# Kernel tuning notes

Hardware: AMD Instinct MI355X
Metric: run time of the kernel (lower is better)

## Reference

```python
import jax, jax.numpy as jnp
import numpy as np

B, T_MEL, E, M, NFPS = 64, 2000, 512, 80, 2
P, H = 256, 1024
T_DEC = T_MEL // NFPS


def setup_inputs() -> dict:
    key = jax.random.key(0)
    ks = iter(jax.random.split(key, 40))

    def rn(shape, fan_in):
        return jax.random.normal(next(ks), shape, jnp.float32) / np.float32(np.sqrt(fan_in))

    z = lambda *s: jnp.zeros(s, jnp.float32)
    return {
        "memorys": jax.random.normal(next(ks), (B, T_MEL, E), jnp.float32),
        "decoder_inputs": jax.random.normal(next(ks), (B, T_MEL, M), jnp.float32),
        "memory_lengths": jax.random.randint(next(ks), (B,), 1, T_MEL + 1),
        "pre_w1": rn((P, M), M), "pre_b1": z(P),
        "pre_w2": rn((P, P), P), "pre_b2": z(P),
        "g1_wih": rn((3 * H, P + E), P + E), "g1_whh": rn((3 * H, H), H),
        "g1_bih": z(3 * H), "g1_bhh": z(3 * H),
        "att_w": rn((H, H + E), H + E), "att_b": z(H),
        "g2_wih": rn((3 * H, H), H), "g2_whh": rn((3 * H, H), H),
        "g2_bih": z(3 * H), "g2_bhh": z(3 * H),
        "g3_wih": rn((3 * H, H), H), "g3_whh": rn((3 * H, H), H),
        "g3_bih": z(3 * H), "g3_bhh": z(3 * H),
        "proj_w": rn((M * NFPS, H + E), H + E), "proj_b": z(M * NFPS),
    }


def gru_cell(x, h, wih, whh, bih, bhh):
    # PyTorch GRUCell gate order: r, z, n
    gi = x @ wih.T + bih
    gh = h @ whh.T + bhh
    i_r, i_z, i_n = jnp.split(gi, 3, axis=-1)
    h_r, h_z, h_n = jnp.split(gh, 3, axis=-1)
    r = jax.nn.sigmoid(i_r + h_r)
    zg = jax.nn.sigmoid(i_z + h_z)
    n = jnp.tanh(i_n + r * h_n)
    return (1.0 - zg) * n + zg * h


def reference(memorys, decoder_inputs, memory_lengths,
              pre_w1, pre_b1, pre_w2, pre_b2,
              g1_wih, g1_whh, g1_bih, g1_bhh,
              att_w, att_b,
              g2_wih, g2_whh, g2_bih, g2_bhh,
              g3_wih, g3_whh, g3_bih, g3_bhh,
              proj_w, proj_b):
    # memory_lengths -> mask is computed but never used in decode(); ignored.
    # Teacher-forced inputs: [T_MEL,B,M] -> every NFPS-th frame, prepend go frames, drop last
    di = jnp.transpose(decoder_inputs, (1, 0, 2))[NFPS - 1::NFPS]   # [T_DEC,B,M]
    go = jnp.zeros((NFPS - 1, B, M), di.dtype)
    di = jnp.concatenate([go, di], axis=0)[:-1]                      # [T_DEC,B,M]
    # Prenet (dropout inactive in deterministic/eval reference)
    x = jax.nn.relu(di @ pre_w1.T + pre_b1)
    x = jax.nn.relu(x @ pre_w2.T + pre_b2)                           # [T_DEC,B,P]
    # Pool memory over n_frames_per_step groups -> per-step context
    mem = memorys.reshape(B, T_DEC, NFPS, E).mean(axis=2)
    mem = jnp.transpose(mem, (1, 0, 2))                              # [T_DEC,B,E]

    def step(carry, inp):
        h1, h2, h3 = carry
        xt, mt = inp
        h1 = gru_cell(jnp.concatenate([xt, mt], -1), h1, g1_wih, g1_whh, g1_bih, g1_bhh)
        d2 = jnp.concatenate([h1, mt], -1) @ att_w.T + att_b
        h2 = gru_cell(d2, h2, g2_wih, g2_whh, g2_bih, g2_bhh)
        r2 = h2 + d2
        h3 = gru_cell(r2, h3, g3_wih, g3_whh, g3_bih, g3_bhh)
        r3 = h3 + r2
        out = jnp.concatenate([r3, mt], -1) @ proj_w.T + proj_b      # [B, M*NFPS]
        return (h1, h2, h3), out

    h0 = tuple(jnp.zeros((B, H), x.dtype) for _ in range(3))
    _, outs = jax.lax.scan(step, h0, (x, mem))                       # [T_DEC,B,M*NFPS]
    return jnp.transpose(outs, (1, 0, 2))                            # [B,T_DEC,M*NFPS]
```

## Files before the change

kernel.cpp:

```cpp
#include <hip/hip_runtime.h>
#include <stdint.h>

#define TD   1000
#define BB   64
#define HH   1024
#define EE   512
#define MMEL 80
#define TMEL 2000
#define RTOT (TD*BB)
#define BH   (BB*HH)
#define DRNG 64

typedef __attribute__((ext_vector_type(8))) short short8;
typedef __attribute__((ext_vector_type(4))) float f32x4;

__device__ __forceinline__ float bf2f(uint16_t h){ return __uint_as_float(((uint32_t)h)<<16); }
__device__ __forceinline__ uint16_t f2bf(float f){
  uint32_t u = __float_as_uint(f);
  return (uint16_t)((u + 0x7fffu + ((u>>16)&1u)) >> 16);
}

__device__ __forceinline__ void async16(const void* g, void* l) {
  __builtin_amdgcn_global_load_lds((const __attribute__((address_space(1))) void*)g,
                                   (__attribute__((address_space(3))) void*)l, 16, 0, 0);
}

__device__ __forceinline__ f32x4 mfma16(short8 a, short8 b, f32x4 c){
  return __builtin_amdgcn_mfma_f32_16x16x32_bf16(a, b, c, 0, 0, 0);
}


__global__ void k_zero16(uint16_t* p, int n){ int i=blockIdx.x*256+threadIdx.x; if(i<n) p[i]=0; }
__global__ void k_zero32(unsigned* p, int n){ int i=blockIdx.x*256+threadIdx.x; if(i<n) p[i]=0u; }
__global__ void k_fill(float* p, int n, float v){ int i=blockIdx.x*256+threadIdx.x; if(i<n) p[i]=v; }

__global__ void k_cast(const float* __restrict__ src, uint16_t* __restrict__ dst,
                       int rows, int src_ld, int col0, int cols, int dst_ld){
  int i = blockIdx.x*256 + threadIdx.x;
  if (i >= rows*dst_ld) return;
  int r = i/dst_ld, c = i - r*dst_ld;
  float v = (c < cols) ? src[(size_t)r*src_ld + col0 + c] : 0.f;
  dst[i] = f2bf(v);
}

__global__ void k_di(const float* __restrict__ dec, uint16_t* __restrict__ di){
  int i = blockIdx.x*256 + threadIdx.x;
  if (i >= RTOT*96) return;
  int row = i/96, c = i - row*96;
  int t = row>>6, b = row&63;
  float v = 0.f;
  if (c < MMEL && t > 0) v = dec[((size_t)b*TMEL + (2*t-1))*MMEL + c];
  di[i] = f2bf(v);
}

__global__ void k_mem(const float* __restrict__ mem, uint16_t* __restrict__ out){
  int i = blockIdx.x*256 + threadIdx.x;
  if (i >= RTOT*EE) return;
  int row = i/EE, e = i - row*EE;
  int t = row>>6, b = row&63;
  size_t base = ((size_t)b*TMEL + 2*t)*EE + e;
  out[i] = f2bf(0.5f*(mem[base] + mem[base+EE]));
}


template<int OM, int DT>
__global__ __launch_bounds__(256)
void k_gemm(const uint16_t* __restrict__ A1p, int K1, int lda1,
            const uint16_t* __restrict__ A2p, int K2, int lda2,
            const uint16_t* __restrict__ Bw, int ldb,
            void* __restrict__ Cp, int ldc,
            const float* __restrict__ bias,
            const void* __restrict__ Dadd, int ldd,
            int N, int relu)
{
  __shared__ __align__(16) uint16_t As[128*32];
  __shared__ __align__(16) uint16_t Bs[128*32];
  const int tid = threadIdx.x;
  const int w = tid>>6, lane = tid&63;
  const int q = lane>>4, ln = lane&15;
  const int m0 = blockIdx.y*128, n0 = blockIdx.x*128;
  const int wr = (w&1)*64, wc = (w>>1)*64;
  const int srow = w*32 + (lane>>2);
  const int scol = (lane&3)*8;
  const uint16_t* A1g = A1p + (size_t)(m0+srow)*lda1 + scol;
  const uint16_t* A1g2 = A1g + (size_t)16*lda1;
  const uint16_t* A2g = A2p ? A2p + (size_t)(m0+srow)*lda2 + scol : nullptr;
  const uint16_t* A2g2 = A2p ? A2g + (size_t)16*lda2 : nullptr;
  int bn1 = n0+srow;     bn1 = bn1 < N ? bn1 : N-1;
  int bn2 = n0+srow+16;  bn2 = bn2 < N ? bn2 : N-1;
  const uint16_t* Bg  = Bw + (size_t)bn1*ldb + scol;
  const uint16_t* Bg2 = Bw + (size_t)bn2*ldb + scol;
  uint16_t* As0 = &As[(w*32)*32];
  uint16_t* As1 = &As[(w*32+16)*32];
  uint16_t* Bs0 = &Bs[(w*32)*32];
  uint16_t* Bs1 = &Bs[(w*32+16)*32];
  const int K = K1 + K2;

  f32x4 acc[4][4] = {};
  for (int kt=0; kt<K; kt+=32) {
    __syncthreads();
    if (kt < K1) { async16(A1g+kt, As0);  async16(A1g2+kt, As1); }
    else         { async16(A2g+(kt-K1), As0);  async16(A2g2+(kt-K1), As1); }
    async16(Bg+kt, Bs0);  async16(Bg2+kt, Bs1);
    __syncthreads();
    short8 af[4], bfr[4];
    #pragma unroll
    for (int i=0;i<4;++i) af[i]  = *(const short8*)&As[(wr+16*i+ln)*32 + q*8];
    #pragma unroll
    for (int j=0;j<4;++j) bfr[j] = *(const short8*)&Bs[(wc+16*j+ln)*32 + q*8];
    #pragma unroll
    for (int i=0;i<4;++i)
      #pragma unroll
      for (int j=0;j<4;++j)
        acc[i][j] = mfma16(af[i], bfr[j], acc[i][j]);
  }

  #pragma unroll
  for (int i=0;i<4;++i){
    #pragma unroll
    for (int j=0;j<4;++j){
      int col = n0 + wc + 16*j + ln;
      if (col >= N) continue;
      float bv = bias ? bias[col] : 0.f;
      #pragma unroll
      for (int r=0;r<4;++r){
        int row = m0 + wr + 16*i + 4*q + r;
        float v = acc[i][j][r] + bv;
        if (Dadd) {
          if (DT) v += ((const float*)Dadd)[(size_t)row*ldd + col];
          else    v += bf2f(((const uint16_t*)Dadd)[(size_t)row*ldd + col]);
        }
        if (relu) v = v > 0.f ? v : 0.f;
        if (OM==0) {
          ((uint16_t*)Cp)[(size_t)row*ldc + col] = f2bf(v);
        } else if (OM==1) {
          int t = row>>6, b = row&63;
          ((float*)Cp)[((size_t)b*TD + t)*ldc + col] = v;
        } else {
          ((float*)Cp)[(size_t)row*ldc + col] = v;
        }
      }
    }
  }
}


__device__ __forceinline__ void signal_flag(unsigned* f, int idx, unsigned v){
  if (threadIdx.x == 0)
    __hip_atomic_store(f + idx*32, v, __ATOMIC_RELEASE, __HIP_MEMORY_SCOPE_AGENT);
}
__device__ __forceinline__ void wait_flags(unsigned* f, int n, unsigned target){
  if ((int)threadIdx.x < n) {
    unsigned* p = f + threadIdx.x*32;
    while (__hip_atomic_load(p, __ATOMIC_RELAXED, __HIP_MEMORY_SCOPE_AGENT) < target)
      __builtin_amdgcn_s_sleep(1);
    __builtin_amdgcn_fence(__ATOMIC_ACQUIRE, "agent");
  }
  __syncthreads();
}


template<int ROLE>
__device__ __forceinline__ void fetch_gi(int t,
    const uint16_t* X2, const uint16_t* MEM, const uint16_t* gsrc,
    const uint16_t* smw, int w, int q, int ln, f32x4 (&ga)[3])
{
  ga[0] = (f32x4){0.f,0.f,0.f,0.f}; ga[1] = ga[0]; ga[2] = ga[0];
  const int swz = (ln&7)<<3;
  if (ROLE == 1) {
    const uint16_t* a0 = X2 + ((size_t)t*64 + 16*w + ln)*256 + q*8;
    #pragma unroll 4
    for (int ks=0; ks<8; ++ks) {
      short8 a = *(const short8*)(a0 + ks*32);
      #pragma unroll
      for (int g=0; g<3; ++g) {
        short8 b = *(const short8*)(smw + ((((g*16+ln)*768) + ks*32 + q*8) ^ swz));
        ga[g] = mfma16(a, b, ga[g]);
      }
    }
    const uint16_t* a1 = MEM + ((size_t)t*64 + 16*w + ln)*512 + q*8;
    #pragma unroll 4
    for (int ks=0; ks<16; ++ks) {
      short8 a = *(const short8*)(a1 + ks*32);
      #pragma unroll
      for (int g=0; g<3; ++g) {
        short8 b = *(const short8*)(smw + ((((g*16+ln)*768) + 256 + ks*32 + q*8) ^ swz));
        ga[g] = mfma16(a, b, ga[g]);
      }
    }
  } else {
    const uint16_t* base = gsrc + (ROLE==2 ? (size_t)(t % DRNG)*BH : (size_t)t*BH);
    const uint16_t* a0 = base + (size_t)(16*w + ln)*1024 + q*8;
    #pragma unroll 8
    for (int ks=0; ks<32; ++ks) {
      short8 a = *(const short8*)(a0 + ks*32);
      #pragma unroll
      for (int g=0; g<3; ++g) {
        short8 b = *(const short8*)(smw + ((((g*16+ln)*1024) + ks*32 + q*8) ^ swz));
        ga[g] = mfma16(a, b, ga[g]);
      }
    }
  }
}


template<int ROLE>
__device__ void rec_role(int i,
    const uint16_t* whh, const uint16_t* wih,
    const float* bih, const float* bhh,
    const uint16_t* X2, const uint16_t* MEM, const uint16_t* gsrc,
    uint16_t* Hs, uint16_t* rout,
    unsigned* fOwn, unsigned* fDep, int nDep,
    uint16_t* smw, float* red)
{
  const int tid = threadIdx.x;
  const int w = tid>>6, lane = tid&63;
  const int q = lane>>4, ln = lane&15;
  const int j = i*16 + ln;
  constexpr int LDK = (ROLE==1) ? 768 : 1024;

  for (int u = tid; u < (48*LDK)/8; u += 256) {
    int row = (u*8)/LDK, col = (u*8) - row*LDK;
    int g = row>>4, r16 = row&15;
    short8 v = *(const short8*)(wih + (size_t)(g*1024 + i*16 + r16)*LDK + col);
    *(short8*)(smw + ((row*LDK + col) ^ ((row&7)<<3))) = v;
  }
  short8 breg[3][8];
  #pragma unroll
  for (int g=0; g<3; ++g) {
    const uint16_t* Bp = whh + (size_t)(g*1024 + j)*1024 + (w*8)*32 + q*8;
    #pragma unroll
    for (int ks=0; ks<8; ++ks) breg[g][ks] = *(const short8*)(Bp + ks*32);
  }
  const float bh0 = bhh[j], bh1 = bhh[1024+j], bh2 = bhh[2048+j];
  const float bi0 = bih[j], bi1 = bih[1024+j], bi2 = bih[2048+j];
  __syncthreads();

  float hold[4] = {0.f,0.f,0.f,0.f};
  f32x4 ga[3];
  if (ROLE != 1) wait_flags(fDep, nDep, 1u);
  fetch_gi<ROLE>(0, X2, MEM, gsrc, smw, w, q, ln, ga);

  for (int t=0; t<TD; ++t) {
    if (t > 0) wait_flags(fOwn, 64, (unsigned)t);
    const uint16_t* hp = Hs + (size_t)t*BH;

    f32x4 acc[3][4];
    #pragma unroll
    for (int g=0; g<3; ++g)
      #pragma unroll
      for (int mt=0; mt<4; ++mt) acc[g][mt] = (f32x4){0.f,0.f,0.f,0.f};
    #pragma unroll
    for (int ks=0; ks<8; ++ks) {
      const int k0 = (w*8+ks)*32 + q*8;
      #pragma unroll
      for (int mt=0; mt<4; ++mt) {
        short8 a = *(const short8*)(hp + (size_t)(16*mt+ln)*HH + k0);
        acc[0][mt] = mfma16(a, breg[0][ks], acc[0][mt]);
        acc[1][mt] = mfma16(a, breg[1][ks], acc[1][mt]);
        acc[2][mt] = mfma16(a, breg[2][ks], acc[2][mt]);
      }
    }
    #pragma unroll
    for (int g=0; g<3; ++g)
      #pragma unroll
      for (int mt=0; mt<4; ++mt)
        *(f32x4*)&red[((w*12 + g*4 + mt)*64 + lane)*4] = acc[g][mt];
    __syncthreads();
    f32x4 s[3];
    #pragma unroll
    for (int g=0; g<3; ++g) {
      f32x4 sv = *(const f32x4*)&red[((g*4 + w)*64 + lane)*4];
      #pragma unroll
      for (int kw=1; kw<4; ++kw)
        sv += *(const f32x4*)&red[((kw*12 + g*4 + w)*64 + lane)*4];
      s[g] = sv;
    }

    const uint16_t* gib = (ROLE==2) ? gsrc + (size_t)(t % DRNG)*BH
                        : (ROLE==3) ? gsrc + (size_t)t*BH : nullptr;
    #pragma unroll
    for (int r=0; r<4; ++r) {
      const int b = 16*w + 4*q + r;
      float rg = 1.f/(1.f + __expf(-(ga[0][r] + bi0 + s[0][r] + bh0)));
      float zg = 1.f/(1.f + __expf(-(ga[1][r] + bi1 + s[1][r] + bh1)));
      float nx = ga[2][r] + bi2 + rg*(s[2][r] + bh2);
      float ng = 1.f - 2.f/(1.f + __expf(2.f*nx));
      float hn = (1.f - zg)*ng + zg*hold[r];
      hold[r] = hn;
      Hs[(size_t)(t+1)*BH + (size_t)b*HH + j] = f2bf(hn);
      if (ROLE != 1) {
        float av = bf2f(gib[(size_t)b*HH + j]);
        rout[((size_t)t*64 + b)*HH + j] = f2bf(hn + av);
      }
    }
    __syncthreads();
    signal_flag(fOwn, i, (unsigned)(t+1));
    if (t+1 < TD) {
      if (ROLE != 1) wait_flags(fDep, nDep, (unsigned)(t+2));
      fetch_gi<ROLE>(t+1, X2, MEM, gsrc, smw, w, q, ln, ga);
    }
  }
}


__device__ void att_role(int i, const uint16_t* wah, const uint16_t* H1,
    const uint16_t* APRE, uint16_t* D2R,
    unsigned* fA, unsigned* fB, unsigned* fD, uint16_t* smw)
{
  const int tid = threadIdx.x;
  const int w = tid>>6, lane = tid&63;
  const int q = lane>>4, ln = lane&15;
  const int c0 = i*32;
  for (int u = tid; u < (32*1024)/8; u += 256) {
    int row = (u*8)>>10, col = (u*8)&1023;
    short8 v = *(const short8*)(wah + (size_t)(c0+row)*1024 + col);
    *(short8*)(smw + ((row*1024 + col) ^ ((row&7)<<3))) = v;
  }
  __syncthreads();
  const int swz = (ln&7)<<3;
  for (int t=0; t<TD; ++t) {
    wait_flags(fA, 64, (unsigned)(t+1));
    if (t >= DRNG) wait_flags(fB, 64, (unsigned)(t - DRNG + 1));
    const uint16_t* h1t = H1 + (size_t)(t+1)*BH;
    f32x4 dacc[2];
    dacc[0] = (f32x4){0.f,0.f,0.f,0.f}; dacc[1] = dacc[0];
    const uint16_t* a0 = h1t + (size_t)(16*w + ln)*HH + q*8;
    #pragma unroll 8
    for (int ks=0; ks<32; ++ks) {
      short8 a = *(const short8*)(a0 + ks*32);
      #pragma unroll
      for (int jf=0; jf<2; ++jf) {
        short8 b = *(const short8*)(smw + ((((jf*16+ln)*1024) + ks*32 + q*8) ^ swz));
        dacc[jf] = mfma16(a, b, dacc[jf]);
      }
    }
    uint16_t* slot = D2R + (size_t)(t % DRNG)*BH;
    #pragma unroll
    for (int jf=0; jf<2; ++jf)
      #pragma unroll
      for (int r=0; r<4; ++r) {
        int b = 16*w + 4*q + r, col = c0 + 16*jf + ln;
        float v = dacc[jf][r] + bf2f(APRE[((size_t)t*64 + b)*HH + col]);
        slot[(size_t)b*HH + col] = f2bf(v);
      }
    __syncthreads();
    signal_flag(fD, i, (unsigned)(t+1));
  }
}


__global__ __launch_bounds__(256,1)
void k_pipe(const uint16_t* wG1WHH, const uint16_t* wG2WHH, const uint16_t* wG3WHH,
            const uint16_t* wG1WIH, const uint16_t* wG2WIH, const uint16_t* wG3WIH,
            const uint16_t* wATTWH,
            const float* b1ih, const float* b1hh, const float* b2ih, const float* b2hh,
            const float* b3ih, const float* b3hh,
            const uint16_t* X2, const uint16_t* MEM, const uint16_t* APRE,
            uint16_t* H1, uint16_t* H2, uint16_t* H3,
            uint16_t* R2, uint16_t* R3, uint16_t* D2R, unsigned* flags)
{
  __shared__ __align__(16) uint16_t smw[49152];
  __shared__ __align__(16) float red[12288];
  unsigned* fA = flags;
  unsigned* fD = flags + 64*32;
  unsigned* fB = flags + 96*32;
  unsigned* fC = flags + 160*32;
  const int blk = blockIdx.x;
  if (blk < 64) {
    rec_role<1>(blk, wG1WHH, wG1WIH, b1ih, b1hh, X2, MEM, nullptr,
                H1, nullptr, fA, nullptr, 0, smw, red);
  } else if (blk < 96) {
    att_role(blk-64, wATTWH, H1, APRE, D2R, fA, fB, fD, smw);
  } else if (blk < 160) {
    rec_role<2>(blk-96, wG2WHH, wG2WIH, b2ih, b2hh, nullptr, nullptr, D2R,
                H2, R2, fB, fD, 32, smw, red);
  } else {
    rec_role<3>(blk-160, wG3WHH, wG3WIH, b3ih, b3hh, nullptr, nullptr, R2,
                H3, R3, fC, fB, 64, smw, red);
  }
}


extern "C" void kernel_launch(void* const* d_in, const int* in_sizes, int n_in,
                              void* d_out, int out_size, void* d_ws, size_t ws_size,
                              hipStream_t stream)
{
  (void)in_sizes; (void)n_in;
  const float* memorys = (const float*)d_in[0];
  const float* decin   = (const float*)d_in[1];
  const float* pre_w1  = (const float*)d_in[3];
  const float* pre_b1  = (const float*)d_in[4];
  const float* pre_w2  = (const float*)d_in[5];
  const float* pre_b2  = (const float*)d_in[6];
  const float* g1_wih  = (const float*)d_in[7];
  const float* g1_whh  = (const float*)d_in[8];
  const float* g1_bih  = (const float*)d_in[9];
  const float* g1_bhh  = (const float*)d_in[10];
  const float* att_w   = (const float*)d_in[11];
  const float* att_b   = (const float*)d_in[12];
  const float* g2_wih  = (const float*)d_in[13];
  const float* g2_whh  = (const float*)d_in[14];
  const float* g2_bih  = (const float*)d_in[15];
  const float* g2_bhh  = (const float*)d_in[16];
  const float* g3_wih  = (const float*)d_in[17];
  const float* g3_whh  = (const float*)d_in[18];
  const float* g3_bih  = (const float*)d_in[19];
  const float* g3_bhh  = (const float*)d_in[20];
  const float* proj_w  = (const float*)d_in[21];
  const float* proj_b  = (const float*)d_in[22];

  uint16_t* ws = (uint16_t*)d_ws;
  size_t off = 0;
  auto alloc = [&](size_t n){ uint16_t* p = ws + off; off += (n + 127) & ~size_t(127); return p; };

  uint16_t* wG1WHH = alloc((size_t)3072*1024);
  uint16_t* wG2WHH = alloc((size_t)3072*1024);
  uint16_t* wG3WHH = alloc((size_t)3072*1024);
  uint16_t* wG1WIH = alloc((size_t)3072*768);
  uint16_t* wG2WIH = alloc((size_t)3072*1024);
  uint16_t* wG3WIH = alloc((size_t)3072*1024);
  uint16_t* wATTWH = alloc((size_t)1024*1024);
  uint16_t* wATTWM = alloc((size_t)1024*512);
  uint16_t* wPW1   = alloc((size_t)256*96);
  uint16_t* wPW2   = alloc((size_t)256*256);
  uint16_t* wPROJr = alloc((size_t)160*1024);
  uint16_t* wPROJm = alloc((size_t)160*512);

  float*    PM   = (float*)alloc((size_t)RTOT*160*2);
  uint16_t* X2   = alloc((size_t)RTOT*256);
  uint16_t* MEM  = alloc((size_t)RTOT*512);
  uint16_t* APRE = alloc((size_t)RTOT*1024);
  uint16_t* H1   = alloc((size_t)(TD+1)*BH);
  uint16_t* H2   = alloc((size_t)(TD+1)*BH);
  uint16_t* H3   = alloc((size_t)(TD+1)*BH);
  uint16_t* R2   = alloc((size_t)RTOT*1024);
  uint16_t* D2R  = alloc((size_t)DRNG*BH);
  unsigned* flags = (unsigned*)(ws + off); off += 224*32*2 + 256;

  uint16_t* DI96 = H3;
  uint16_t* X1   = H2;

  size_t need_bytes = off * 2;
  if (ws_size < need_bytes) {
    float v = 1048576.0f + (float)(ws_size >> 20);
    k_fill<<<dim3((out_size+255)/256), dim3(256), 0, stream>>>((float*)d_out, out_size, v);
    return;
  }

  auto NB = [](long long n){ return dim3((unsigned)((n+255)/256)); };

  k_cast<<<NB(3072*1024), dim3(256), 0, stream>>>(g1_whh, wG1WHH, 3072, 1024, 0, 1024, 1024);
  k_cast<<<NB(3072*1024), dim3(256), 0, stream>>>(g2_whh, wG2WHH, 3072, 1024, 0, 1024, 1024);
  k_cast<<<NB(3072*1024), dim3(256), 0, stream>>>(g3_whh, wG3WHH, 3072, 1024, 0, 1024, 1024);
  k_cast<<<NB(3072*768),  dim3(256), 0, stream>>>(g1_wih, wG1WIH, 3072, 768, 0, 768, 768);
  k_cast<<<NB(3072*1024), dim3(256), 0, stream>>>(g2_wih, wG2WIH, 3072, 1024, 0, 1024, 1024);
  k_cast<<<NB(3072*1024), dim3(256), 0, stream>>>(g3_wih, wG3WIH, 3072, 1024, 0, 1024, 1024);
  k_cast<<<NB(1024*1024), dim3(256), 0, stream>>>(att_w,  wATTWH, 1024, 1536, 0, 1024, 1024);
  k_cast<<<NB(1024*512),  dim3(256), 0, stream>>>(att_w,  wATTWM, 1024, 1536, 1024, 512, 512);
  k_cast<<<NB(256*96),    dim3(256), 0, stream>>>(pre_w1, wPW1,   256, 80, 0, 80, 96);
  k_cast<<<NB(256*256),   dim3(256), 0, stream>>>(pre_w2, wPW2,   256, 256, 0, 256, 256);
  k_cast<<<NB(160*1024),  dim3(256), 0, stream>>>(proj_w, wPROJr, 160, 1536, 0, 1024, 1024);
  k_cast<<<NB(160*512),   dim3(256), 0, stream>>>(proj_w, wPROJm, 160, 1536, 1024, 512, 512);

  k_di <<<NB((long long)RTOT*96),  dim3(256), 0, stream>>>(decin, DI96);
  k_mem<<<NB((long long)RTOT*EE),  dim3(256), 0, stream>>>(memorys, MEM);

  k_gemm<0,0><<<dim3(2,500), dim3(256), 0, stream>>>(DI96,96,96, nullptr,0,0, wPW1,96, X1,256, pre_b1, nullptr,0, 256, 1);
  k_gemm<0,0><<<dim3(2,500), dim3(256), 0, stream>>>(X1,256,256, nullptr,0,0, wPW2,256, X2,256, pre_b2, nullptr,0, 256, 1);

  k_gemm<0,0><<<dim3(8,500), dim3(256), 0, stream>>>(MEM,512,512, nullptr,0,0, wATTWM,512, APRE,1024, att_b, nullptr,0, 1024, 0);
  k_gemm<2,0><<<dim3(2,500), dim3(256), 0, stream>>>(MEM,512,512, nullptr,0,0, wPROJm,512, PM,160, proj_b, nullptr,0, 160, 0);

  k_zero16<<<NB(BH), dim3(256), 0, stream>>>(H1, BH);
  k_zero16<<<NB(BH), dim3(256), 0, stream>>>(H2, BH);
  k_zero16<<<NB(BH), dim3(256), 0, stream>>>(H3, BH);
  k_zero32<<<dim3(28), dim3(256), 0, stream>>>(flags, 224*32);

  k_pipe<<<dim3(224), dim3(256), 0, stream>>>(
      wG1WHH, wG2WHH, wG3WHH, wG1WIH, wG2WIH, wG3WIH, wATTWH,
      g1_bih, g1_bhh, g2_bih, g2_bhh, g3_bih, g3_bhh,
      X2, MEM, APRE, H1, H2, H3, R2, APRE, D2R, flags);

  k_gemm<1,1><<<dim3(2,500), dim3(256), 0, stream>>>(APRE,1024,1024, nullptr,0,0, wPROJr,1024, d_out,160, nullptr, PM,160, 160, 0);
}
```

Measured before the change: 16.95 ms.

## Precompute GRU1 input gates, ring-buffer hidden states, batch bypass loads

The GRU1 input projection (prenet output plus memory context times W_ih) moves out of the persistent recurrent kernel into one large upfront GEMM, so layer-1 blocks only read precomputed gates each step. Hidden-state and residual histories become small ring buffers, with backpressure flags so producers cannot overwrite slots their consumers have not read yet. A combined wait routine checks both own-progress and downstream flags, and operand loads are batched through relaxed atomic loads that bypass the cache. This is meant to shorten the serial per-step critical path and cut memory footprint. The cost is an extra GI1 buffer and more complex cross-block synchronisation, which raises deadlock and ordering risk; the acquire fence after waiting was also dropped.

Result: slower. 23.81 ms (+40.5%).

```diff
diff --git a/kernel.cpp b/kernel.cpp
--- a/kernel.cpp
+++ b/kernel.cpp
@@ -9,10 +9,13 @@
 #define TMEL 2000
 #define RTOT (TD*BB)
 #define BH   (BB*HH)
-#define DRNG 64
+#define RH1  80
+#define RH23 8
+#define RNG  64
 
 typedef __attribute__((ext_vector_type(8))) short short8;
 typedef __attribute__((ext_vector_type(4))) float f32x4;
+typedef unsigned long long u64t;
 
 __device__ __forceinline__ float bf2f(uint16_t h){ return __uint_as_float(((uint32_t)h)<<16); }
 __device__ __forceinline__ uint16_t f2bf(float f){
@@ -27,6 +30,12 @@
 
 __device__ __forceinline__ f32x4 mfma16(short8 a, short8 b, f32x4 c){
   return __builtin_amdgcn_mfma_f32_16x16x32_bf16(a, b, c, 0, 0, 0);
+}
+
+__device__ __forceinline__ short8 ld16_bypass(const uint16_t* p){
+  u64t lo = __hip_atomic_load((const u64t*)p,       __ATOMIC_RELAXED, __HIP_MEMORY_SCOPE_AGENT);
+  u64t hi = __hip_atomic_load(((const u64t*)p) + 1, __ATOMIC_RELAXED, __HIP_MEMORY_SCOPE_AGENT);
+  union { u64t q[2]; short8 s; } u; u.q[0] = lo; u.q[1] = hi; return u.s;
 }
 
 
@@ -149,81 +158,70 @@
   if (threadIdx.x == 0)
     __hip_atomic_store(f + idx*32, v, __ATOMIC_RELEASE, __HIP_MEMORY_SCOPE_AGENT);
 }
-__device__ __forceinline__ void wait_flags(unsigned* f, int n, unsigned target){
-  if ((int)threadIdx.x < n) {
-    unsigned* p = f + threadIdx.x*32;
-    while (__hip_atomic_load(p, __ATOMIC_RELAXED, __HIP_MEMORY_SCOPE_AGENT) < target)
+
+__device__ __forceinline__ void wait2(unsigned* f0, int n0, unsigned t0,
+                                      unsigned* f1, int n1, unsigned t1){
+  const int tid = threadIdx.x;
+  unsigned* p = nullptr; unsigned tgt = 0;
+  if (tid < n0)            { p = f0 + tid*32;       tgt = t0; }
+  else if (tid < n0 + n1)  { p = f1 + (tid-n0)*32;  tgt = t1; }
+  if (p && tgt)
+    while (__hip_atomic_load(p, __ATOMIC_RELAXED, __HIP_MEMORY_SCOPE_AGENT) < tgt)
       __builtin_amdgcn_s_sleep(1);
-    __builtin_amdgcn_fence(__ATOMIC_ACQUIRE, "agent");
-  }
   __syncthreads();
 }
 
 
 template<int ROLE>
-__device__ __forceinline__ void fetch_gi(int t,
-    const uint16_t* X2, const uint16_t* MEM, const uint16_t* gsrc,
-    const uint16_t* smw, int w, int q, int ln, f32x4 (&ga)[3])
+__device__ __forceinline__ void fetch_tail(int t, const uint16_t* gsrc,
+    const uint16_t* smw, int w, int q, int ln, int j, f32x4 (&ga)[3], float (&gibv)[4])
 {
+  const uint16_t* base = gsrc + (size_t)(t & (RNG-1))*BH;
   ga[0] = (f32x4){0.f,0.f,0.f,0.f}; ga[1] = ga[0]; ga[2] = ga[0];
   const int swz = (ln&7)<<3;
-  if (ROLE == 1) {
-    const uint16_t* a0 = X2 + ((size_t)t*64 + 16*w + ln)*256 + q*8;
-    #pragma unroll 4
-    for (int ks=0; ks<8; ++ks) {
-      short8 a = *(const short8*)(a0 + ks*32);
-      #pragma unroll
-      for (int g=0; g<3; ++g) {
-        short8 b = *(const short8*)(smw + ((((g*16+ln)*768) + ks*32 + q*8) ^ swz));
-        ga[g] = mfma16(a, b, ga[g]);
-      }
-    }
-    const uint16_t* a1 = MEM + ((size_t)t*64 + 16*w + ln)*512 + q*8;
-    #pragma unroll 4
-    for (int ks=0; ks<16; ++ks) {
-      short8 a = *(const short8*)(a1 + ks*32);
-      #pragma unroll
-      for (int g=0; g<3; ++g) {
-        short8 b = *(const short8*)(smw + ((((g*16+ln)*768) + 256 + ks*32 + q*8) ^ swz));
-        ga[g] = mfma16(a, b, ga[g]);
-      }
-    }
-  } else {
-    const uint16_t* base = gsrc + (ROLE==2 ? (size_t)(t % DRNG)*BH : (size_t)t*BH);
-    const uint16_t* a0 = base + (size_t)(16*w + ln)*1024 + q*8;
-    #pragma unroll 8
-    for (int ks=0; ks<32; ++ks) {
-      short8 a = *(const short8*)(a0 + ks*32);
-      #pragma unroll
-      for (int g=0; g<3; ++g) {
-        short8 b = *(const short8*)(smw + ((((g*16+ln)*1024) + ks*32 + q*8) ^ swz));
-        ga[g] = mfma16(a, b, ga[g]);
-      }
-    }
+  short8 a2[32];
+  #pragma unroll
+  for (int ks=0; ks<32; ++ks)
+    a2[ks] = ld16_bypass(base + (size_t)(16*w+ln)*1024 + q*8 + ks*32);
+  #pragma unroll
+  for (int ks=0; ks<32; ++ks) {
+    #pragma unroll
+    for (int g=0; g<3; ++g) {
+      short8 b = *(const short8*)(smw + ((((g*16+ln)*1024) + ks*32 + q*8) ^ swz));
+      ga[g] = mfma16(a2[ks], b, ga[g]);
+    }
+  }
+  #pragma unroll
+  for (int r=0; r<4; ++r){
+    int b = 16*w + 4*q + r;
+    unsigned v = __hip_atomic_load((const unsigned*)(base + (size_t)b*HH + (j & ~1)),
+                                   __ATOMIC_RELAXED, __HIP_MEMORY_SCOPE_AGENT);
+    gibv[r] = bf2f((uint16_t)((j&1) ? (v>>16) : (v & 0xffffu)));
   }
 }
 
 
 template<int ROLE>
 __device__ void rec_role(int i,
-    const uint16_t* whh, const uint16_t* wih,
-    const float* bih, const float* bhh,
-    const uint16_t* X2, const uint16_t* MEM, const uint16_t* gsrc,
-    uint16_t* Hs, uint16_t* rout,
-    unsigned* fOwn, unsigned* fDep, int nDep,
+    const uint16_t* __restrict__ whh, const uint16_t* __restrict__ wih,
+    const float* __restrict__ bih, const float* __restrict__ bhh,
+    const uint16_t* __restrict__ GI1, const uint16_t* __restrict__ gsrc,
+    uint16_t* __restrict__ Hs, uint16_t* __restrict__ rout,
+    unsigned* fOwn, unsigned* fPrev, int nPrev, unsigned* fNext, int nNext,
     uint16_t* smw, float* red)
 {
   const int tid = threadIdx.x;
   const int w = tid>>6, lane = tid&63;
   const int q = lane>>4, ln = lane&15;
   const int j = i*16 + ln;
-  constexpr int LDK = (ROLE==1) ? 768 : 1024;
-
-  for (int u = tid; u < (48*LDK)/8; u += 256) {
-    int row = (u*8)/LDK, col = (u*8) - row*LDK;
-    int g = row>>4, r16 = row&15;
-    short8 v = *(const short8*)(wih + (size_t)(g*1024 + i*16 + r16)*LDK + col);
-    *(short8*)(smw + ((row*LDK + col) ^ ((row&7)<<3))) = v;
+  constexpr int RH = (ROLE==1) ? RH1 : RH23;
+
+  if (ROLE != 1) {
+    for (int u = tid; u < (48*1024)/8; u += 256) {
+      int row = (u*8)>>10, col = (u*8)&1023;
+      short8 v = *(const short8*)(wih + (size_t)((row>>4)*1024 + i*16 + (row&15))*1024 + col);
+      *(short8*)(smw + ((row*1024 + col) ^ ((row&7)<<3))) = v;
+    }
   }
   short8 breg[3][8];
   #pragma unroll
@@ -233,17 +231,40 @@
     for (int ks=0; ks<8; ++ks) breg[g][ks] = *(const short8*)(Bp + ks*32);
   }
   const float bh0 = bhh[j], bh1 = bhh[1024+j], bh2 = bhh[2048+j];
-  const float bi0 = bih[j], bi1 = bih[1024+j], bi2 = bih[2048+j];
+  float bi0 = 0.f, bi1 = 0.f, bi2 = 0.f;
+  if (ROLE != 1) { bi0 = bih[j]; bi1 = bih[1024+j]; bi2 = bih[2048+j]; }
   __syncthreads();
 
   float hold[4] = {0.f,0.f,0.f,0.f};
   f32x4 ga[3];
-  if (ROLE != 1) wait_flags(fDep, nDep, 1u);
-  fetch_gi<ROLE>(0, X2, MEM, gsrc, smw, w, q, ln, ga);
+  float gibv[4] = {0.f,0.f,0.f,0.f};
+
+  if (ROLE == 1) {
+    #pragma unroll
+    for (int r=0; r<4; ++r){
+      size_t gb = (size_t)(16*w + 4*q + r)*3072;
+      ga[0][r] = bf2f(GI1[gb + j]);
+      ga[1][r] = bf2f(GI1[gb + 1024 + j]);
+      ga[2][r] = bf2f(GI1[gb + 2048 + j]);
+    }
+  } else {
+    wait2(fPrev, nPrev, 1u, nullptr, 0, 0u);
+    fetch_tail<ROLE>(0, gsrc, smw, w, q, ln, j, ga, gibv);
+  }
 
   for (int t=0; t<TD; ++t) {
-    if (t > 0) wait_flags(fOwn, 64, (unsigned)t);
-    const uint16_t* hp = Hs + (size_t)t*BH;
+    unsigned bp = 0u;
+    if (ROLE == 1)      bp = (t >= RH1-1) ? (unsigned)(t - (RH1-2)) : 0u;
+    else if (nNext)     bp = (t >= RNG)   ? (unsigned)(t - (RNG-1)) : 0u;
+    wait2(fOwn, 64, (unsigned)t, fNext, nNext, bp);
+
+    const uint16_t* hp = Hs + (size_t)(t % RH)*BH;
+    short8 av[32];
+    #pragma unroll
+    for (int ks=0; ks<8; ++ks)
+      #pragma unroll
+      for (int mt=0; mt<4; ++mt)
+        av[ks*4+mt] = ld16_bypass(hp + (size_t)(16*mt+ln)*HH + (w*8+ks)*32 + q*8);
 
     f32x4 acc[3][4];
     #pragma unroll
@@ -252,15 +273,14 @@
       for (int mt=0; mt<4; ++mt) acc[g][mt] = (f32x4){0.f,0.f,0.f,0.f};
     #pragma unroll
     for (int ks=0; ks<8; ++ks) {
-      const int k0 = (w*8+ks)*32 + q*8;
       #pragma unroll
       for (int mt=0; mt<4; ++mt) {
-        short8 a = *(const short8*)(hp + (size_t)(16*mt+ln)*HH + k0);
-        acc[0][mt] = mfma16(a, breg[0][ks], acc[0][mt]);
-        acc[1][mt] = mfma16(a, breg[1][ks], acc[1][mt]);
-        acc[2][mt] = mfma16(a, breg[2][ks], acc[2][mt]);
+        acc[0][mt] = mfma16(av[ks*4+mt], breg[0][ks], acc[0][mt]);
+        acc[1][mt] = mfma16(av[ks*4+mt], breg[1][ks], acc[1][mt]);
+        acc[2][mt] = mfma16(av[ks*4+mt], breg[2][ks], acc[2][mt]);
       }
     }
+
     #pragma unroll
     for (int g=0; g<3; ++g)
       #pragma unroll
@@ -277,8 +297,7 @@
       s[g] = sv;
     }
 
-    const uint16_t* gib = (ROLE==2) ? gsrc + (size_t)(t % DRNG)*BH
-                        : (ROLE==3) ? gsrc + (size_t)t*BH : nullptr;
+    uint16_t* hw = Hs + (size_t)((t+1) % RH)*BH;
     #pragma unroll
     for (int r=0; r<4; ++r) {
       const int b = 16*w + 4*q + r;
@@ -288,25 +307,35 @@
       float ng = 1.f - 2.f/(1.f + __expf(2.f*nx));
       float hn = (1.f - zg)*ng + zg*hold[r];
       hold[r] = hn;
-      Hs[(size_t)(t+1)*BH + (size_t)b*HH + j] = f2bf(hn);
-      if (ROLE != 1) {
-        float av = bf2f(gib[(size_t)b*HH + j]);
-        rout[((size_t)t*64 + b)*HH + j] = f2bf(hn + av);
-      }
+      hw[(size_t)b*HH + j] = f2bf(hn);
+      if (ROLE == 2) rout[(size_t)(t & (RNG-1))*BH + (size_t)b*HH + j] = f2bf(hn + gibv[r]);
+      if (ROLE == 3) rout[((size_t)t*64 + b)*HH + j] = f2bf(hn + gibv[r]);
     }
     __syncthreads();
     signal_flag(fOwn, i, (unsigned)(t+1));
+
     if (t+1 < TD) {
-      if (ROLE != 1) wait_flags(fDep, nDep, (unsigned)(t+2));
-      fetch_gi<ROLE>(t+1, X2, MEM, gsrc, smw, w, q, ln, ga);
-    }
-  }
-}
-
-
-__device__ void att_role(int i, const uint16_t* wah, const uint16_t* H1,
-    const uint16_t* APRE, uint16_t* D2R,
-    unsigned* fA, unsigned* fB, unsigned* fD, uint16_t* smw)
+      if (ROLE == 1) {
+        #pragma unroll
+        for (int r=0; r<4; ++r){
+          size_t gb = ((size_t)(t+1)*64 + 16*w + 4*q + r)*3072;
+          ga[0][r] = bf2f(GI1[gb + j]);
+          ga[1][r] = bf2f(GI1[gb + 1024 + j]);
+          ga[2][r] = bf2f(GI1[gb + 2048 + j]);
+        }
+      } else {
+        wait2(fPrev, nPrev, (unsigned)(t+2), nullptr, 0, 0u);
+        fetch_tail<ROLE>(t+1, gsrc, smw, w, q, ln, j, ga, gibv);
+      }
+    }
+  }
+}
+
+
+__device__ void att_role(int i, const uint16_t* __restrict__ wah,
+    const uint16_t* __restrict__ H1, const uint16_t* __restrict__ APRE,
+    uint16_t* __restrict__ D2R, unsigned* fA, unsigned* fB, unsigned* fD,
+    uint16_t* smw)
 {
   const int tid = threadIdx.x;
   const int w = tid>>6, lane = tid&63;
@@ -320,29 +349,38 @@
   __syncthreads();
   const int swz = (ln&7)<<3;
   for (int t=0; t<TD; ++t) {
-    wait_flags(fA, 64, (unsigned)(t+1));
-    if (t >= DRNG) wait_flags(fB, 64, (unsigned)(t - DRNG + 1));
-    const uint16_t* h1t = H1 + (size_t)(t+1)*BH;
+    float apv[2][4];
+    #pragma unroll
+    for (int jf=0; jf<2; ++jf)
+      #pragma unroll
+      for (int r=0; r<4; ++r)
+        apv[jf][r] = bf2f(APRE[((size_t)t*64 + 16*w + 4*q + r)*HH + c0 + 16*jf + ln]);
+
+    unsigned bp = (t >= RNG) ? (unsigned)(t - (RNG-1)) : 0u;
+    wait2(fA, 64, (unsigned)(t+1), fB, 64, bp);
+
+    const uint16_t* h1t = H1 + (size_t)((t+1) % RH1)*BH;
+    short8 av[32];
+    #pragma unroll
+    for (int ks=0; ks<32; ++ks)
+      av[ks] = ld16_bypass(h1t + (size_t)(16*w+ln)*HH + q*8 + ks*32);
     f32x4 dacc[2];
     dacc[0] = (f32x4){0.f,0.f,0.f,0.f}; dacc[1] = dacc[0];
-    const uint16_t* a0 = h1t + (size_t)(16*w + ln)*HH + q*8;
-    #pragma unroll 8
+    #pragma unroll
     for (int ks=0; ks<32; ++ks) {
-      short8 a = *(const short8*)(a0 + ks*32);
       #pragma unroll
       for (int jf=0; jf<2; ++jf) {
         short8 b = *(const short8*)(smw + ((((jf*16+ln)*1024) + ks*32 + q*8) ^ swz));
-        dacc[jf] = mfma16(a, b, dacc[jf]);
+        dacc[jf] = mfma16(av[ks], b, dacc[jf]);
       }
     }
-    uint16_t* slot = D2R + (size_t)(t % DRNG)*BH;
+    uint16_t* slot = D2R + (size_t)(t & (RNG-1))*BH;
     #pragma unroll
     for (int jf=0; jf<2; ++jf)
       #pragma unroll
       for (int r=0; r<4; ++r) {
-        int b = 16*w + 4*q + r, col = c0 + 16*jf + ln;
-        float v = dacc[jf][r] + bf2f(APRE[((size_t)t*64 + b)*HH + col]);
-        slot[(size_t)b*HH + col] = f2bf(v);
+        int b = 16*w + 4*q + r;
+        slot[(size_t)b*HH + c0 + 16*jf + ln] = f2bf(dacc[jf][r] + apv[jf][r]);
       }
     __syncthreads();
     signal_flag(fD, i, (unsigned)(t+1));
@@ -352,11 +390,10 @@
 
 __global__ __launch_bounds__(256,1)
 void k_pipe(const uint16_t* wG1WHH, const uint16_t* wG2WHH, const uint16_t* wG3WHH,
-            const uint16_t* wG1WIH, const uint16_t* wG2WIH, const uint16_t* wG3WIH,
-            const uint16_t* wATTWH,
-            const float* b1ih, const float* b1hh, const float* b2ih, const float* b2hh,
+            const uint16_t* wG2WIH, const uint16_t* wG3WIH, const uint16_t* wATTWH,
+            const float* b1hh, const float* b2ih, const float* b2hh,
             const float* b3ih, const float* b3hh,
-            const uint16_t* X2, const uint16_t* MEM, const uint16_t* APRE,
+            const uint16_t* GI1, const uint16_t* APRE,
             uint16_t* H1, uint16_t* H2, uint16_t* H3,
             uint16_t* R2, uint16_t* R3, uint16_t* D2R, unsigned* flags)
 {
@@ -367,18 +404,17 @@
   unsigned* fB = flags + 96*32;
   unsigned* fC = flags + 160*32;
   const int blk = blockIdx.x;
-  if (blk < 64) {
-    rec_role<1>(blk, wG1WHH, wG1WIH, b1ih, b1hh, X2, MEM, nullptr,
-                H1, nullptr, fA, nullptr, 0, smw, red);
-  } else if (blk < 96) {
+  if (blk < 64)
+    rec_role<1>(blk, wG1WHH, nullptr, nullptr, b1hh, GI1, nullptr, H1, nullptr,
+                fA, nullptr, 0, fD, 32, smw, red);
+  else if (blk < 96)
     att_role(blk-64, wATTWH, H1, APRE, D2R, fA, fB, fD, smw);
-  } else if (blk < 160) {
-    rec_role<2>(blk-96, wG2WHH, wG2WIH, b2ih, b2hh, nullptr, nullptr, D2R,
-                H2, R2, fB, fD, 32, smw, red);
-  } else {
-    rec_role<3>(blk-160, wG3WHH, wG3WIH, b3ih, b3hh, nullptr, nullptr, R2,
-                H3, R3, fC, fB, 64, smw, red);
-  }
+  else if (blk < 160)
+    rec_role<2>(blk-96, wG2WHH, wG2WIH, b2ih, b2hh, nullptr, D2R, H2, R2,
+                fB, fD, 32, fC, 64, smw, red);
+  else
+    rec_role<3>(blk-160, wG3WHH, wG3WIH, b3ih, b3hh, nullptr, R2, H3, R3,
+                fC, fB, 64, nullptr, 0, smw, red);
 }
 
 
@@ -431,15 +467,16 @@
   uint16_t* X2   = alloc((size_t)RTOT*256);
   uint16_t* MEM  = alloc((size_t)RTOT*512);
   uint16_t* APRE = alloc((size_t)RTOT*1024);
-  uint16_t* H1   = alloc((size_t)(TD+1)*BH);
-  uint16_t* H2   = alloc((size_t)(TD+1)*BH);
-  uint16_t* H3   = alloc((size_t)(TD+1)*BH);
-  uint16_t* R2   = alloc((size_t)RTOT*1024);
-  uint16_t* D2R  = alloc((size_t)DRNG*BH);
+  uint16_t* GI1  = alloc((size_t)RTOT*3072);
+  uint16_t* H1   = alloc((size_t)RH1*BH);
+  uint16_t* H2   = alloc((size_t)RH23*BH);
+  uint16_t* H3   = alloc((size_t)RH23*BH);
+  uint16_t* R2   = alloc((size_t)RNG*BH);
+  uint16_t* D2R  = alloc((size_t)RNG*BH);
   unsigned* flags = (unsigned*)(ws + off); off += 224*32*2 + 256;
 
-  uint16_t* DI96 = H3;
-  uint16_t* X1   = H2;
+  uint16_t* DI96 = GI1;
+  uint16_t* X1   = GI1 + (size_t)RTOT*96;
 
   size_t need_bytes = off * 2;
   if (ws_size < need_bytes) {
@@ -469,6 +506,7 @@
   k_gemm<0,0><<<dim3(2,500), dim3(256), 0, stream>>>(DI96,96,96, nullptr,0,0, wPW1,96, X1,256, pre_b1, nullptr,0, 256, 1);
   k_gemm<0,0><<<dim3(2,500), dim3(256), 0, stream>>>(X1,256,256, nullptr,0,0, wPW2,256, X2,256, pre_b2, nullptr,0, 256, 1);
 
+  k_gemm<0,0><<<dim3(24,500), dim3(256), 0, stream>>>(X2,256,256, MEM,512,512, wG1WIH,768, GI1,3072, g1_bih, nullptr,0, 3072, 0);
   k_gemm<0,0><<<dim3(8,500), dim3(256), 0, stream>>>(MEM,512,512, nullptr,0,0, wATTWM,512, APRE,1024, att_b, nullptr,0, 1024, 0);
   k_gemm<2,0><<<dim3(2,500), dim3(256), 0, stream>>>(MEM,512,512, nullptr,0,0, wPROJm,512, PM,160, proj_b, nullptr,0, 160, 0);
 
@@ -478,9 +516,9 @@
   k_zero32<<<dim3(28), dim3(256), 0, stream>>>(flags, 224*32);
 
   k_pipe<<<dim3(224), dim3(256), 0, stream>>>(
-      wG1WHH, wG2WHH, wG3WHH, wG1WIH, wG2WIH, wG3WIH, wATTWH,
-      g1_bih, g1_bhh, g2_bih, g2_bhh, g3_bih, g3_bhh,
-      X2, MEM, APRE, H1, H2, H3, R2, APRE, D2R, flags);
+      wG1WHH, wG2WHH, wG3WHH, wG2WIH, wG3WIH, wATTWH,
+      g1_bhh, g2_bih, g2_bhh, g3_bih, g3_bhh,
+      GI1, APRE, H1, H2, H3, R2, APRE, D2R, flags);
 
   k_gemm<1,1><<<dim3(2,500), dim3(256), 0, stream>>>(APRE,1024,1024, nullptr,0,0, wPROJr,1024, d_out,160, nullptr, PM,160, 160, 0);
 }
```
